# Kernel optimization log

Hardware: AMD Instinct MI355X
Metric: run time of the kernel (lower is better)

## Reference

```python
import jax, jax.numpy as jnp
import numpy as np

NEG_INF = -1e9  # matches masked_fill value in the torch source


def setup_inputs() -> dict:
    key0 = jax.random.key(0)
    kq, kk, kv, km = jax.random.split(key0, 4)
    B, H, S, D = 2, 12, 2048, 64
    query = jax.random.normal(kq, (B, H, S, D), dtype=jnp.float32)
    key = jax.random.normal(kk, (B, H, S, D), dtype=jnp.float32)
    value = jax.random.normal(kv, (B, H, S, D), dtype=jnp.float32)
    mask = jax.random.randint(km, (B, S, S), 0, 2, dtype=jnp.int32)
    return {"query": query, "key": key, "value": value, "mask": mask}


def reference(query, key, value, mask):
    # query/key/value: [B, H, S, D]; mask: [B, S, S] (0 = masked out)
    d = key.shape[-1]
    scale = 1.0 / np.sqrt(d).astype(np.float32)
    # attn scores: [B, H, Sq, Sk]
    attn = jnp.einsum("bhqd,bhkd->bhqk", query * scale, key)
    m = mask[:, None, :, :]  # broadcast over heads, mirrors mask.unsqueeze(1)
    attn = jnp.where(m == 0, jnp.float32(NEG_INF), attn)
    attn = jax.nn.softmax(attn, axis=-1)
    # dropout_ratio = 0.0 -> identity
    out = jnp.einsum("bhqk,bhkd->bhqd", attn, value)
    return out
```

## Files before the change

kernel.cpp:

```cpp
#include <hip/hip_runtime.h>

#define SQ 2048
#define DH 64
#define NH 12
#define NBH 24

typedef __attribute__((ext_vector_type(8))) short short8;
typedef __attribute__((ext_vector_type(4))) float f32x4;

union U8 { uint4 u; short8 s; };

__device__ __forceinline__ unsigned short f2bf(float x) {
  union { float f; unsigned u; } v; v.f = x;
  return (unsigned short)((v.u + 0x7FFFu + ((v.u >> 16) & 1u)) >> 16);
}

__device__ __forceinline__ unsigned pk2(float a, float b) {
  unsigned ua = __builtin_bit_cast(unsigned, a) + 0x8000u;
  unsigned ub = __builtin_bit_cast(unsigned, b) + 0x8000u;
  return __builtin_amdgcn_perm(ub, ua, 0x07060302);
}

__device__ __forceinline__ void gload_lds16(const void* g, void* l) {
  __builtin_amdgcn_global_load_lds(
      (const __attribute__((address_space(1))) unsigned*)g,
      (__attribute__((address_space(3))) unsigned*)l, 16, 0, 0);
}

__global__ __launch_bounds__(256) void prep_all(
    const float* __restrict__ Q, const float* __restrict__ K,
    const float* __restrict__ V, const int* __restrict__ M,
    unsigned short* __restrict__ Qb, unsigned short* __restrict__ Kb,
    unsigned short* __restrict__ Vt, unsigned* __restrict__ mbits) {
  const int bid = blockIdx.x, tid = threadIdx.x;
  if (bid < 3072) {
    int i = bid * 256 + tid;
    float4 q = ((const float4*)Q)[i];
    float4 k = ((const float4*)K)[i];
    const float sc = 0.125f * 1.44269504f;
    ushort4 qo, ko;
    qo.x = f2bf(q.x * sc); qo.y = f2bf(q.y * sc);
    qo.z = f2bf(q.z * sc); qo.w = f2bf(q.w * sc);
    ko.x = f2bf(k.x); ko.y = f2bf(k.y); ko.z = f2bf(k.z); ko.w = f2bf(k.w);
    ((ushort4*)Qb)[i] = qo;
    ((ushort4*)Kb)[i] = ko;
  } else if (bid < 3840) {
    __shared__ float T[64 * 65];
    int bx = bid - 3072;
    int bh = bx >> 5, st = bx & 31;
    int s0 = st * 64;
    int c4 = (tid & 15) * 4, r0 = tid >> 4;
#pragma unroll
    for (int it = 0; it < 4; ++it) {
      int r = r0 + 16 * it;
      float4 v = *(const float4*)(V + ((size_t)(bh * SQ + s0 + r)) * DH + c4);
      T[r * 65 + c4 + 0] = v.x; T[r * 65 + c4 + 1] = v.y;
      T[r * 65 + c4 + 2] = v.z; T[r * 65 + c4 + 3] = v.w;
    }
    __syncthreads();
#pragma unroll
    for (int it = 0; it < 2; ++it) {
      int cc = tid + 256 * it;
      int d = cc >> 3, c8 = (cc & 7) * 8;
      short8 o;
#pragma unroll
      for (int j = 0; j < 8; ++j) o[j] = (short)f2bf(T[(c8 + j) * 65 + d]);
      *(short8*)(Vt + ((size_t)(bh * 64 + d)) * SQ + s0 + c8) = o;
    }
  } else {
    int w = tid >> 6, lane = tid & 63;
    int row = (bid - 3840) * 4 + w;
    const int* mrow = M + (size_t)row * SQ;
    unsigned long long out = 0;
#pragma unroll
    for (int j = 0; j < 32; ++j) {
      int mv = mrow[j * 64 + lane];
      unsigned long long bits = __ballot(mv != 0);
      if (lane == j) out = bits;
    }
    if (lane < 32)
      ((unsigned long long*)mbits)[(size_t)row * 32 + lane] = out;
  }
}

__global__ __launch_bounds__(256, 3) void attn_kernel(
    const unsigned short* __restrict__ Qb, const unsigned short* __restrict__ Kb,
    const unsigned short* __restrict__ Vt, const unsigned* __restrict__ mbits,
    float* __restrict__ O0, float* __restrict__ O1, float* __restrict__ Lp) {
  __shared__ uint4 FIFO[2][16][64];

  const int bx = blockIdx.x;
  const int bh = bx % NBH;
  const int rest = bx / NBH;
  const int qt = rest & 15, ks = rest >> 4;
  const int b = bh / NH;
  const int tid = threadIdx.x;
  const int lane = tid & 63, w = tid >> 6;
  const int m = lane & 15, quad = lane >> 4;
  const int q0 = qt * 128 + w * 32;

  short8 qf[2][2];
#pragma unroll
  for (int g = 0; g < 2; ++g) {
    const unsigned short* qp = Qb + ((size_t)(bh * SQ + q0 + g * 16 + m)) * DH + quad * 8;
    qf[g][0] = *(const short8*)qp;
    qf[g][1] = *(const short8*)(qp + 32);
  }

  const unsigned short* gp[4];
  if (w < 2) {
#pragma unroll
    for (int j = 0; j < 4; ++j) {
      int chunk = w * 4 + j;
      int t = chunk >> 1, h = chunk & 1;
      int row = ks * (SQ / 2) + 32 * (t >> 1) + 4 * (t & 1) + 8 * (m >> 2) + (m & 3);
      gp[j] = Kb + ((size_t)bh * SQ + row) * DH + 32 * h + 8 * quad;
    }
  } else {
#pragma unroll
    for (int j = 0; j < 4; ++j) {
      int cid = (w - 2) * 4 + j;
      int c = cid >> 2, dt = cid & 3;
      gp[j] = Vt + ((size_t)bh * DH + dt * 16 + m) * SQ + ks * (SQ / 2) + 32 * c + 8 * quad;
    }
  }
  const int gstride = (w < 2) ? 64 * DH : 64;
  const int chunk0 = w * 4;

  const unsigned long long* mp0 =
      (const unsigned long long*)mbits + ((size_t)b * SQ + q0 + m) * 32 + ks * 16;
  const unsigned long long* mp1 = mp0 + (size_t)16 * 32;

  short8 ones;
#pragma unroll
  for (int j = 0; j < 8; ++j) ones[j] = (short)0x3F80;

  f32x4 acc[2][4], sumac[2];
#pragma unroll
  for (int g = 0; g < 2; ++g) {
    sumac[g] = (f32x4){0.f, 0.f, 0.f, 0.f};
#pragma unroll
    for (int dt = 0; dt < 4; ++dt) acc[g][dt] = (f32x4){0.f, 0.f, 0.f, 0.f};
  }

#pragma unroll
  for (int j = 0; j < 4; ++j) {
    gload_lds16(gp[j], &FIFO[0][chunk0 + j][0]);
    gp[j] += gstride;
  }
  __syncthreads();

  for (int nt = 0; nt < 16; ++nt) {
    const int cur = nt & 1;
    if (nt < 15) {
#pragma unroll
      for (int j = 0; j < 4; ++j) {
        gload_lds16(gp[j], &FIFO[1 - cur][chunk0 + j][0]);
        gp[j] += gstride;
      }
    }
    unsigned long long mc0 = *mp0, mc1 = *mp1;
    ++mp0; ++mp1;

    f32x4 st[2][4];
#pragma unroll
    for (int t = 0; t < 4; ++t) {
      U8 k0, k1;
      k0.u = FIFO[cur][t * 2 + 0][lane];
      k1.u = FIFO[cur][t * 2 + 1][lane];
#pragma unroll
      for (int g = 0; g < 2; ++g) {
        f32x4 a = (f32x4){0.f, 0.f, 0.f, 0.f};
        a = __builtin_amdgcn_mfma_f32_16x16x32_bf16(k0.s, qf[g][0], a, 0, 0, 0);
        a = __builtin_amdgcn_mfma_f32_16x16x32_bf16(k1.s, qf[g][1], a, 0, 0, 0);
        st[g][t] = a;
      }
    }

    short8 pb[2][2];
#pragma unroll
    for (int g = 0; g < 2; ++g) {
      unsigned long long mg = g ? mc1 : mc0;
      unsigned w0 = (unsigned)mg, w1 = (unsigned)(mg >> 32);
      unsigned by0 = (w0 >> (quad * 8)) & 0xFFu;
      unsigned by1 = (w1 >> (quad * 8)) & 0xFFu;
      float p[4][4];
#pragma unroll
      for (int t = 0; t < 4; ++t) {
        unsigned byt = (t < 2) ? by0 : by1;
#pragma unroll
        for (int r = 0; r < 4; ++r) {
          float e = __builtin_amdgcn_exp2f(st[g][t][r]);
          p[t][r] = ((byt >> (4 * (t & 1) + r)) & 1u) ? e : 0.f;
        }
      }
      U8 x0, x1;
      x0.u = (uint4){pk2(p[0][0], p[0][1]), pk2(p[0][2], p[0][3]),
                     pk2(p[1][0], p[1][1]), pk2(p[1][2], p[1][3])};
      x1.u = (uint4){pk2(p[2][0], p[2][1]), pk2(p[2][2], p[2][3]),
                     pk2(p[3][0], p[3][1]), pk2(p[3][2], p[3][3])};
      pb[g][0] = x0.s;
      pb[g][1] = x1.s;
    }

#pragma unroll
    for (int g = 0; g < 2; ++g) {
      sumac[g] = __builtin_amdgcn_mfma_f32_16x16x32_bf16(ones, pb[g][0], sumac[g], 0, 0, 0);
      sumac[g] = __builtin_amdgcn_mfma_f32_16x16x32_bf16(ones, pb[g][1], sumac[g], 0, 0, 0);
    }

#pragma unroll
    for (int c = 0; c < 2; ++c)
#pragma unroll
      for (int dt = 0; dt < 4; ++dt) {
        U8 x; x.u = FIFO[cur][8 + c * 4 + dt][lane];
#pragma unroll
        for (int g = 0; g < 2; ++g)
          acc[g][dt] = __builtin_amdgcn_mfma_f32_16x16x32_bf16(x.s, pb[g][c], acc[g][dt], 0, 0, 0);
      }

    __syncthreads();
  }

  float* Op = ks ? O1 : O0;
#pragma unroll
  for (int g = 0; g < 2; ++g) {
    float* op = Op + ((size_t)(bh * SQ + q0 + g * 16 + m)) * DH + quad * 4;
#pragma unroll
    for (int dt = 0; dt < 4; ++dt) {
      float4 o = {acc[g][dt][0], acc[g][dt][1], acc[g][dt][2], acc[g][dt][3]};
      *(float4*)(op + dt * 16) = o;
    }
    if (quad == 0) Lp[(size_t)ks * NBH * SQ + bh * SQ + q0 + g * 16 + m] = sumac[g][0];
  }
}

__global__ __launch_bounds__(256) void combine(float* __restrict__ Out,
                                               const float* __restrict__ O1,
                                               const float* __restrict__ Lp) {
  int i = blockIdx.x * 256 + threadIdx.x;
  float4 a = ((const float4*)Out)[i];
  float4 b = ((const float4*)O1)[i];
  int q = i >> 4;
  float inv = __builtin_amdgcn_rcpf(Lp[q] + Lp[NBH * SQ + q]);
  float4 o = {(a.x + b.x) * inv, (a.y + b.y) * inv,
              (a.z + b.z) * inv, (a.w + b.w) * inv};
  ((float4*)Out)[i] = o;
}

extern "C" void kernel_launch(void* const* d_in, const int* in_sizes, int n_in,
                              void* d_out, int out_size, void* d_ws, size_t ws_size,
                              hipStream_t stream) {
  const float* Q = (const float*)d_in[0];
  const float* K = (const float*)d_in[1];
  const float* V = (const float*)d_in[2];
  const int*   M = (const int*)d_in[3];
  float* Out = (float*)d_out;

  size_t NB = (size_t)NBH * SQ * DH;
  unsigned short* Qb = (unsigned short*)d_ws;
  unsigned short* Kb = Qb + NB;
  unsigned short* Vt = Kb + NB;
  unsigned* mbits = (unsigned*)(Vt + NB);
  float* O1 = (float*)(mbits + (size_t)2 * SQ * 64);
  float* Lp = O1 + NB;

  prep_all<<<4864, 256, 0, stream>>>(Q, K, V, M, Qb, Kb, Vt, mbits);
  attn_kernel<<<NBH * 16 * 2, 256, 0, stream>>>(Qb, Kb, Vt, mbits, Out, O1, Lp);
  combine<<<(int)(NB / 4 / 256), 256, 0, stream>>>(Out, O1, Lp);
}
```

Baseline: 159.9 us.

## Split keys four ways when workspace allows, restructure score loop per group

The key dimension is split into a runtime number of segments, four when the workspace is large enough and otherwise two, so the attention grid grows from 768 to 1536 blocks. Partial outputs and row sums go to extra workspace and the combine kernel sums all segments. The score loop now computes scores for each query group right before its exp, which shortens register live ranges, and launch bounds rise to 4 waves per SIMD for more occupancy. The cost is more partial-output traffic in combine, a runtime loop bound in place of a fixed count, and a risk of register spills under the tighter bound.

Measured after the change: 167.2 us. 4.6% more time.

```diff
diff --git a/kernel.cpp b/kernel.cpp
--- a/kernel.cpp
+++ b/kernel.cpp
@@ -83,10 +83,11 @@
   }
 }
 
-__global__ __launch_bounds__(256, 3) void attn_kernel(
+__global__ __launch_bounds__(256, 4) void attn_kernel(
     const unsigned short* __restrict__ Qb, const unsigned short* __restrict__ Kb,
     const unsigned short* __restrict__ Vt, const unsigned* __restrict__ mbits,
-    float* __restrict__ O0, float* __restrict__ O1, float* __restrict__ Lp) {
+    float* __restrict__ O0, float* __restrict__ Opart, float* __restrict__ Lp,
+    int nks, int iters) {
   __shared__ uint4 FIFO[2][16][64];
 
   const int bx = blockIdx.x;
@@ -98,6 +99,7 @@
   const int lane = tid & 63, w = tid >> 6;
   const int m = lane & 15, quad = lane >> 4;
   const int q0 = qt * 128 + w * 32;
+  const int k0 = ks * (SQ / nks) ;
 
   short8 qf[2][2];
 #pragma unroll
@@ -113,7 +115,7 @@
     for (int j = 0; j < 4; ++j) {
       int chunk = w * 4 + j;
       int t = chunk >> 1, h = chunk & 1;
-      int row = ks * (SQ / 2) + 32 * (t >> 1) + 4 * (t & 1) + 8 * (m >> 2) + (m & 3);
+      int row = k0 + 32 * (t >> 1) + 4 * (t & 1) + 8 * (m >> 2) + (m & 3);
       gp[j] = Kb + ((size_t)bh * SQ + row) * DH + 32 * h + 8 * quad;
     }
   } else {
@@ -121,14 +123,14 @@
     for (int j = 0; j < 4; ++j) {
       int cid = (w - 2) * 4 + j;
       int c = cid >> 2, dt = cid & 3;
-      gp[j] = Vt + ((size_t)bh * DH + dt * 16 + m) * SQ + ks * (SQ / 2) + 32 * c + 8 * quad;
+      gp[j] = Vt + ((size_t)bh * DH + dt * 16 + m) * SQ + k0 + 32 * c + 8 * quad;
     }
   }
   const int gstride = (w < 2) ? 64 * DH : 64;
   const int chunk0 = w * 4;
 
   const unsigned long long* mp0 =
-      (const unsigned long long*)mbits + ((size_t)b * SQ + q0 + m) * 32 + ks * 16;
+      (const unsigned long long*)mbits + ((size_t)b * SQ + q0 + m) * 32 + (k0 >> 6);
   const unsigned long long* mp1 = mp0 + (size_t)16 * 32;
 
   short8 ones;
@@ -150,9 +152,9 @@
   }
   __syncthreads();
 
-  for (int nt = 0; nt < 16; ++nt) {
+  for (int nt = 0; nt < iters; ++nt) {
     const int cur = nt & 1;
-    if (nt < 15) {
+    if (nt < iters - 1) {
 #pragma unroll
       for (int j = 0; j < 4; ++j) {
         gload_lds16(gp[j], &FIFO[1 - cur][chunk0 + j][0]);
@@ -162,24 +164,20 @@
     unsigned long long mc0 = *mp0, mc1 = *mp1;
     ++mp0; ++mp1;
 
-    f32x4 st[2][4];
-#pragma unroll
-    for (int t = 0; t < 4; ++t) {
-      U8 k0, k1;
-      k0.u = FIFO[cur][t * 2 + 0][lane];
-      k1.u = FIFO[cur][t * 2 + 1][lane];
-#pragma unroll
-      for (int g = 0; g < 2; ++g) {
+    short8 pb[2][2];
+#pragma unroll
+    for (int g = 0; g < 2; ++g) {
+      f32x4 stg[4];
+#pragma unroll
+      for (int t = 0; t < 4; ++t) {
+        U8 k0f, k1f;
+        k0f.u = FIFO[cur][t * 2 + 0][lane];
+        k1f.u = FIFO[cur][t * 2 + 1][lane];
         f32x4 a = (f32x4){0.f, 0.f, 0.f, 0.f};
-        a = __builtin_amdgcn_mfma_f32_16x16x32_bf16(k0.s, qf[g][0], a, 0, 0, 0);
-        a = __builtin_amdgcn_mfma_f32_16x16x32_bf16(k1.s, qf[g][1], a, 0, 0, 0);
-        st[g][t] = a;
-      }
-    }
-
-    short8 pb[2][2];
-#pragma unroll
-    for (int g = 0; g < 2; ++g) {
+        a = __builtin_amdgcn_mfma_f32_16x16x32_bf16(k0f.s, qf[g][0], a, 0, 0, 0);
+        a = __builtin_amdgcn_mfma_f32_16x16x32_bf16(k1f.s, qf[g][1], a, 0, 0, 0);
+        stg[t] = a;
+      }
       unsigned long long mg = g ? mc1 : mc0;
       unsigned w0 = (unsigned)mg, w1 = (unsigned)(mg >> 32);
       unsigned by0 = (w0 >> (quad * 8)) & 0xFFu;
@@ -190,7 +188,7 @@
         unsigned byt = (t < 2) ? by0 : by1;
 #pragma unroll
         for (int r = 0; r < 4; ++r) {
-          float e = __builtin_amdgcn_exp2f(st[g][t][r]);
+          float e = __builtin_amdgcn_exp2f(stg[t][r]);
           p[t][r] = ((byt >> (4 * (t & 1) + r)) & 1u) ? e : 0.f;
         }
       }
@@ -222,7 +220,7 @@
     __syncthreads();
   }
 
-  float* Op = ks ? O1 : O0;
+  float* Op = ks ? (Opart + (size_t)(ks - 1) * NBH * SQ * DH) : O0;
 #pragma unroll
   for (int g = 0; g < 2; ++g) {
     float* op = Op + ((size_t)(bh * SQ + q0 + g * 16 + m)) * DH + quad * 4;
@@ -236,15 +234,20 @@
 }
 
 __global__ __launch_bounds__(256) void combine(float* __restrict__ Out,
-                                               const float* __restrict__ O1,
-                                               const float* __restrict__ Lp) {
+                                               const float* __restrict__ Opart,
+                                               const float* __restrict__ Lp,
+                                               int nks) {
   int i = blockIdx.x * 256 + threadIdx.x;
   float4 a = ((const float4*)Out)[i];
-  float4 b = ((const float4*)O1)[i];
   int q = i >> 4;
-  float inv = __builtin_amdgcn_rcpf(Lp[q] + Lp[NBH * SQ + q]);
-  float4 o = {(a.x + b.x) * inv, (a.y + b.y) * inv,
-              (a.z + b.z) * inv, (a.w + b.w) * inv};
+  float l = Lp[q];
+  for (int j = 1; j < nks; ++j) {
+    float4 p = ((const float4*)Opart)[(size_t)(j - 1) * (NBH * SQ * DH / 4) + i];
+    a.x += p.x; a.y += p.y; a.z += p.z; a.w += p.w;
+    l += Lp[(size_t)j * NBH * SQ + q];
+  }
+  float inv = __builtin_amdgcn_rcpf(l);
+  float4 o = {a.x * inv, a.y * inv, a.z * inv, a.w * inv};
   ((float4*)Out)[i] = o;
 }
 
@@ -262,10 +265,14 @@
   unsigned short* Kb = Qb + NB;
   unsigned short* Vt = Kb + NB;
   unsigned* mbits = (unsigned*)(Vt + NB);
-  float* O1 = (float*)(mbits + (size_t)2 * SQ * 64);
-  float* Lp = O1 + NB;
+  float* Opart = (float*)(mbits + (size_t)2 * SQ * 64);
+
+  size_t base = 3 * NB * 2 + (size_t)2 * SQ * 64 * 4;
+  int nks = (ws_size >= base + 3 * NB * 4 + (size_t)4 * NBH * SQ * 4 + 1024) ? 4 : 2;
+  float* Lp = Opart + (size_t)(nks - 1) * NB;
 
   prep_all<<<4864, 256, 0, stream>>>(Q, K, V, M, Qb, Kb, Vt, mbits);
-  attn_kernel<<<NBH * 16 * 2, 256, 0, stream>>>(Qb, Kb, Vt, mbits, Out, O1, Lp);
-  combine<<<(int)(NB / 4 / 256), 256, 0, stream>>>(Out, O1, Lp);
-}
+  attn_kernel<<<NBH * 16 * nks, 256, 0, stream>>>(Qb, Kb, Vt, mbits, Out, Opart, Lp,
+                                                  nks, (SQ / 64) / nks);
+  combine<<<(int)(NB / 4 / 256), 256, 0, stream>>>(Out, Opart, Lp, nks);
+}
```

## Switch attention MFMAs from 16x16x32 to 32x32x16 bf16 tiles

Applied to the files above, without the earlier changes.

Rewrites the attention kernel's QK^T, row-sum and PV matrix ops to use 32x32x16 bf16 MFMA instructions instead of 16x16x32. The K and V LDS fragment layouts, the mask-bit extraction and the output write-back are remapped to the 32-lane row layout, with a bit swizzle on K rows. The aim is fewer MFMA issues and fragment reads per tile and better operand reuse. In exchange, 16-wide accumulators raise register pressure, which may affect occupancy under the 3-blocks-per-CU launch bound.

After: 157.3 us. About the same (-1.6%).

```diff
diff --git a/kernel.cpp b/kernel.cpp
--- a/kernel.cpp
+++ b/kernel.cpp
@@ -6,7 +6,7 @@
 #define NBH 24
 
 typedef __attribute__((ext_vector_type(8))) short short8;
-typedef __attribute__((ext_vector_type(4))) float f32x4;
+typedef __attribute__((ext_vector_type(16))) float f32x16;
 
 union U8 { uint4 u; short8 s; };
 
@@ -25,6 +25,10 @@
   __builtin_amdgcn_global_load_lds(
       (const __attribute__((address_space(1))) unsigned*)g,
       (__attribute__((address_space(3))) unsigned*)l, 16, 0, 0);
+}
+
+__device__ __forceinline__ int sw23(int x) {
+  return (x & 19) | ((x & 4) << 1) | ((x & 8) >> 1);
 }
 
 __global__ __launch_bounds__(256) void prep_all(
@@ -96,52 +100,43 @@
   const int b = bh / NH;
   const int tid = threadIdx.x;
   const int lane = tid & 63, w = tid >> 6;
-  const int m = lane & 15, quad = lane >> 4;
-  const int q0 = qt * 128 + w * 32;
-
-  short8 qf[2][2];
-#pragma unroll
-  for (int g = 0; g < 2; ++g) {
-    const unsigned short* qp = Qb + ((size_t)(bh * SQ + q0 + g * 16 + m)) * DH + quad * 8;
-    qf[g][0] = *(const short8*)qp;
-    qf[g][1] = *(const short8*)(qp + 32);
-  }
+  const int n = lane & 31, h = lane >> 5;
+  const int qrow = qt * 128 + w * 32 + n;
+  const int k0 = ks * (SQ / 2);
+
+  short8 qf[4];
+#pragma unroll
+  for (int s = 0; s < 4; ++s)
+    qf[s] = *(const short8*)(Qb + ((size_t)(bh * SQ + qrow)) * DH + 16 * s + 8 * h);
 
   const unsigned short* gp[4];
   if (w < 2) {
 #pragma unroll
     for (int j = 0; j < 4; ++j) {
-      int chunk = w * 4 + j;
-      int t = chunk >> 1, h = chunk & 1;
-      int row = ks * (SQ / 2) + 32 * (t >> 1) + 4 * (t & 1) + 8 * (m >> 2) + (m & 3);
-      gp[j] = Kb + ((size_t)bh * SQ + row) * DH + 32 * h + 8 * quad;
+      int c = 4 * w + j;
+      int row = k0 + 32 * (c >> 2) + sw23(n);
+      gp[j] = Kb + ((size_t)bh * SQ + row) * DH + 16 * (c & 3) + 8 * h;
     }
   } else {
 #pragma unroll
     for (int j = 0; j < 4; ++j) {
-      int cid = (w - 2) * 4 + j;
-      int c = cid >> 2, dt = cid & 3;
-      gp[j] = Vt + ((size_t)bh * DH + dt * 16 + m) * SQ + ks * (SQ / 2) + 32 * c + 8 * quad;
+      int cc = 4 * (w - 2) + j;
+      gp[j] = Vt + ((size_t)bh * DH + 32 * (cc >> 2) + n) * SQ + k0 + 16 * (cc & 3) + 8 * h;
     }
   }
   const int gstride = (w < 2) ? 64 * DH : 64;
   const int chunk0 = w * 4;
 
-  const unsigned long long* mp0 =
-      (const unsigned long long*)mbits + ((size_t)b * SQ + q0 + m) * 32 + ks * 16;
-  const unsigned long long* mp1 = mp0 + (size_t)16 * 32;
+  const unsigned long long* mp =
+      (const unsigned long long*)mbits + ((size_t)b * SQ + qrow) * 32 + (k0 >> 6);
 
   short8 ones;
 #pragma unroll
   for (int j = 0; j < 8; ++j) ones[j] = (short)0x3F80;
 
-  f32x4 acc[2][4], sumac[2];
-#pragma unroll
-  for (int g = 0; g < 2; ++g) {
-    sumac[g] = (f32x4){0.f, 0.f, 0.f, 0.f};
-#pragma unroll
-    for (int dt = 0; dt < 4; ++dt) acc[g][dt] = (f32x4){0.f, 0.f, 0.f, 0.f};
-  }
+  f32x16 acc0 = {0,0,0,0,0,0,0,0,0,0,0,0,0,0,0,0};
+  f32x16 acc1 = {0,0,0,0,0,0,0,0,0,0,0,0,0,0,0,0};
+  f32x16 sumac = {0,0,0,0,0,0,0,0,0,0,0,0,0,0,0,0};
 
 #pragma unroll
   for (int j = 0; j < 4; ++j) {
@@ -159,80 +154,57 @@
         gp[j] += gstride;
       }
     }
-    unsigned long long mc0 = *mp0, mc1 = *mp1;
-    ++mp0; ++mp1;
-
-    f32x4 st[2][4];
-#pragma unroll
-    for (int t = 0; t < 4; ++t) {
-      U8 k0, k1;
-      k0.u = FIFO[cur][t * 2 + 0][lane];
-      k1.u = FIFO[cur][t * 2 + 1][lane];
-#pragma unroll
-      for (int g = 0; g < 2; ++g) {
-        f32x4 a = (f32x4){0.f, 0.f, 0.f, 0.f};
-        a = __builtin_amdgcn_mfma_f32_16x16x32_bf16(k0.s, qf[g][0], a, 0, 0, 0);
-        a = __builtin_amdgcn_mfma_f32_16x16x32_bf16(k1.s, qf[g][1], a, 0, 0, 0);
-        st[g][t] = a;
+    unsigned long long mg = *mp; ++mp;
+
+    short8 pb[2][2];
+#pragma unroll
+    for (int u = 0; u < 2; ++u) {
+      f32x16 st = {0,0,0,0,0,0,0,0,0,0,0,0,0,0,0,0};
+#pragma unroll
+      for (int s = 0; s < 4; ++s) {
+        U8 kf; kf.u = FIFO[cur][4 * u + s][lane];
+        st = __builtin_amdgcn_mfma_f32_32x32x16_bf16(kf.s, qf[s], st, 0, 0, 0);
       }
-    }
-
-    short8 pb[2][2];
-#pragma unroll
-    for (int g = 0; g < 2; ++g) {
-      unsigned long long mg = g ? mc1 : mc0;
-      unsigned w0 = (unsigned)mg, w1 = (unsigned)(mg >> 32);
-      unsigned by0 = (w0 >> (quad * 8)) & 0xFFu;
-      unsigned by1 = (w1 >> (quad * 8)) & 0xFFu;
-      float p[4][4];
-#pragma unroll
-      for (int t = 0; t < 4; ++t) {
-        unsigned byt = (t < 2) ? by0 : by1;
-#pragma unroll
-        for (int r = 0; r < 4; ++r) {
-          float e = __builtin_amdgcn_exp2f(st[g][t][r]);
-          p[t][r] = ((byt >> (4 * (t & 1) + r)) & 1u) ? e : 0.f;
-        }
+      unsigned blo = (unsigned)(mg >> (8 * (4 * u + h))) & 0xFFu;
+      unsigned bhi = (unsigned)(mg >> (8 * (4 * u + 2 + h))) & 0xFFu;
+      float p[16];
+#pragma unroll
+      for (int j = 0; j < 16; ++j) {
+        float e = __builtin_amdgcn_exp2f(st[j]);
+        unsigned byt = (j < 8) ? blo : bhi;
+        p[j] = ((byt >> (j & 7)) & 1u) ? e : 0.f;
       }
       U8 x0, x1;
-      x0.u = (uint4){pk2(p[0][0], p[0][1]), pk2(p[0][2], p[0][3]),
-                     pk2(p[1][0], p[1][1]), pk2(p[1][2], p[1][3])};
-      x1.u = (uint4){pk2(p[2][0], p[2][1]), pk2(p[2][2], p[2][3]),
-                     pk2(p[3][0], p[3][1]), pk2(p[3][2], p[3][3])};
-      pb[g][0] = x0.s;
-      pb[g][1] = x1.s;
-    }
-
-#pragma unroll
-    for (int g = 0; g < 2; ++g) {
-      sumac[g] = __builtin_amdgcn_mfma_f32_16x16x32_bf16(ones, pb[g][0], sumac[g], 0, 0, 0);
-      sumac[g] = __builtin_amdgcn_mfma_f32_16x16x32_bf16(ones, pb[g][1], sumac[g], 0, 0, 0);
-    }
-
-#pragma unroll
-    for (int c = 0; c < 2; ++c)
-#pragma unroll
-      for (int dt = 0; dt < 4; ++dt) {
-        U8 x; x.u = FIFO[cur][8 + c * 4 + dt][lane];
-#pragma unroll
-        for (int g = 0; g < 2; ++g)
-          acc[g][dt] = __builtin_amdgcn_mfma_f32_16x16x32_bf16(x.s, pb[g][c], acc[g][dt], 0, 0, 0);
-      }
+      x0.u = (uint4){pk2(p[0], p[1]), pk2(p[2], p[3]), pk2(p[4], p[5]), pk2(p[6], p[7])};
+      x1.u = (uint4){pk2(p[8], p[9]), pk2(p[10], p[11]), pk2(p[12], p[13]), pk2(p[14], p[15])};
+      pb[u][0] = x0.s;
+      pb[u][1] = x1.s;
+    }
+
+#pragma unroll
+    for (int t = 0; t < 4; ++t) {
+      short8 pf = pb[t >> 1][t & 1];
+      sumac = __builtin_amdgcn_mfma_f32_32x32x16_bf16(ones, pf, sumac, 0, 0, 0);
+      U8 v0; v0.u = FIFO[cur][8 + t][lane];
+      acc0 = __builtin_amdgcn_mfma_f32_32x32x16_bf16(v0.s, pf, acc0, 0, 0, 0);
+      U8 v1; v1.u = FIFO[cur][12 + t][lane];
+      acc1 = __builtin_amdgcn_mfma_f32_32x32x16_bf16(v1.s, pf, acc1, 0, 0, 0);
+    }
 
     __syncthreads();
   }
 
-  float* Op = ks ? O1 : O0;
-#pragma unroll
-  for (int g = 0; g < 2; ++g) {
-    float* op = Op + ((size_t)(bh * SQ + q0 + g * 16 + m)) * DH + quad * 4;
-#pragma unroll
-    for (int dt = 0; dt < 4; ++dt) {
-      float4 o = {acc[g][dt][0], acc[g][dt][1], acc[g][dt][2], acc[g][dt][3]};
-      *(float4*)(op + dt * 16) = o;
-    }
-    if (quad == 0) Lp[(size_t)ks * NBH * SQ + bh * SQ + q0 + g * 16 + m] = sumac[g][0];
-  }
+  float* op = (ks ? O1 : O0) + ((size_t)(bh * SQ + qrow)) * DH;
+#pragma unroll
+  for (int dt = 0; dt < 2; ++dt) {
+    f32x16 A = dt ? acc1 : acc0;
+#pragma unroll
+    for (int a = 0; a < 4; ++a) {
+      float4 o = {A[4 * a], A[4 * a + 1], A[4 * a + 2], A[4 * a + 3]};
+      *(float4*)(op + 32 * dt + 8 * a + 4 * h) = o;
+    }
+  }
+  if (lane < 32) Lp[(size_t)ks * NBH * SQ + bh * SQ + qrow] = sumac[0];
 }
 
 __global__ __launch_bounds__(256) void combine(float* __restrict__ Out,
@@ -240,11 +212,11 @@
                                                const float* __restrict__ Lp) {
   int i = blockIdx.x * 256 + threadIdx.x;
   float4 a = ((const float4*)Out)[i];
-  float4 b = ((const float4*)O1)[i];
+  float4 bb = ((const float4*)O1)[i];
   int q = i >> 4;
   float inv = __builtin_amdgcn_rcpf(Lp[q] + Lp[NBH * SQ + q]);
-  float4 o = {(a.x + b.x) * inv, (a.y + b.y) * inv,
-              (a.z + b.z) * inv, (a.w + b.w) * inv};
+  float4 o = {(a.x + bb.x) * inv, (a.y + bb.y) * inv,
+              (a.z + bb.z) * inv, (a.w + bb.w) * inv};
   ((float4*)Out)[i] = o;
 }
 
```
